# Kernel tuning notes

Measured on AMD Instinct MI355X. Metric: run time of the kernel, lower is better.

Reference implementation:

```python
import jax, jax.numpy as jnp
import numpy as np

N_NODES = 50000
N_EDGES = 1_600_000
IN_DIM = 256
OUT_DIM = 128
NEG_SLOPE = 0.01  # F.leaky_relu default


def setup_inputs() -> dict:
    key = jax.random.key(0)
    k1, k2, k3, k4, k5 = jax.random.split(key, 5)
    x = jax.random.normal(k1, (N_NODES, IN_DIM), dtype=jnp.float32)
    # glorot_init: uniform in [-r, r], r = sqrt(6/(in+out))
    r = np.sqrt(6.0 / (IN_DIM + OUT_DIM)).astype(np.float32)
    weight = jax.random.uniform(k2, (IN_DIM, OUT_DIM), dtype=jnp.float32, minval=-r, maxval=r)
    adj_rows = jax.random.randint(k3, (N_EDGES,), 0, N_NODES, dtype=jnp.int64 if jax.config.jax_enable_x64 else jnp.int32)
    adj_cols = jax.random.randint(k4, (N_EDGES,), 0, N_NODES, dtype=jnp.int64 if jax.config.jax_enable_x64 else jnp.int32)
    adj_vals = jax.random.uniform(k5, (N_EDGES,), dtype=jnp.float32)
    return {"x": x, "weight": weight, "adj_vals": adj_vals,
            "adj_rows": adj_rows, "adj_cols": adj_cols}


def reference(x, weight, adj_vals, adj_rows, adj_cols):
    # h = X @ W : [N, OUT_DIM]
    h = x @ weight
    # sparse adj @ h via edge-list SpMM: out[r] += v * h[c]
    msgs = adj_vals[:, None] * h[adj_cols]            # [E, OUT_DIM]
    agg = jax.ops.segment_sum(msgs, adj_rows, num_segments=N_NODES)
    # leaky_relu epilogue
    return jnp.where(agg >= 0, agg, NEG_SLOPE * agg)
```

## Files before the change

kernel.cpp:

```cpp
#include <hip/hip_runtime.h>
#include <hip/hip_fp16.h>

#define N_NODES 50000
#define N_EDGES 1600000
#define IN_DIM 256
#define OUT_DIM 128
#define NEG_SLOPE 0.01f

#define BIN_SH    7
#define BIN_ROWS  128
#define NBIN      ((N_NODES + BIN_ROWS - 1) / BIN_ROWS)
#define CAPB      4864

#define HIST_BLOCKS 512
#define CONVW_BLOCKS 16
#define EPB_H (N_EDGES / HIST_BLOCKS)
#define SCAT_BLOCKS 512
#define EPB_S (N_EDGES / SCAT_BLOCKS)
#define SCAT_ITERS ((EPB_S + 511) / 512)

typedef _Float16 f16x8 __attribute__((ext_vector_type(8)));
typedef float    f32x4 __attribute__((ext_vector_type(4)));
typedef float    f32x8 __attribute__((ext_vector_type(8)));

__device__ __forceinline__ float lrelu(float v) {
    return v >= 0.f ? v : NEG_SLOPE * v;
}

#define BM 128
#define GEMM_BLOCKS ((N_NODES + BM - 1) / BM)

#define CVT16(lo, hi) do { \
    lo[0]=(_Float16)xr[0].x; lo[1]=(_Float16)xr[0].y; lo[2]=(_Float16)xr[0].z; lo[3]=(_Float16)xr[0].w; \
    lo[4]=(_Float16)xr[1].x; lo[5]=(_Float16)xr[1].y; lo[6]=(_Float16)xr[1].z; lo[7]=(_Float16)xr[1].w; \
    hi[0]=(_Float16)xr[2].x; hi[1]=(_Float16)xr[2].y; hi[2]=(_Float16)xr[2].z; hi[3]=(_Float16)xr[2].w; \
    hi[4]=(_Float16)xr[3].x; hi[5]=(_Float16)xr[3].y; hi[6]=(_Float16)xr[3].z; hi[7]=(_Float16)xr[3].w; \
} while (0)

__global__ __launch_bounds__(256, 2) void gemm_xw_mfma(const float* __restrict__ x,
                                                       const __half* __restrict__ wtl,
                                                       __half* __restrict__ h) {
    __shared__ f16x8 wt8[32 * 128];
    __shared__ f16x8 xs8[2][4][BM];

    const int t    = threadIdx.x;
    const int lane = t & 63;
    const int wv   = t >> 6;
    const int row0 = blockIdx.x * BM;

    {
        const int4* src = (const int4*)wtl;
        int4* dst = (int4*)wt8;
#pragma unroll
        for (int i = 0; i < 16; ++i) dst[i * 256 + t] = src[i * 256 + t];
    }

    const int srow = t >> 1;
    const int skh  = t & 1;
    const int grow = row0 + srow;
    const bool rv  = grow < N_NODES;
    const float* xp = x + (size_t)(rv ? grow : 0) * IN_DIM + skh * 16;

    float4 xr[4];
#pragma unroll
    for (int i = 0; i < 4; ++i)
        xr[i] = rv ? ((const float4*)xp)[i] : make_float4(0.f, 0.f, 0.f, 0.f);
    {
        f16x8 lo, hi;
        CVT16(lo, hi);
        xs8[0][skh * 2 + 0][srow] = lo;
        xs8[0][skh * 2 + 1][srow] = hi;
    }
    __syncthreads();

    f32x4 acc[2][8];
#pragma unroll
    for (int mf = 0; mf < 2; ++mf)
#pragma unroll
        for (int nf = 0; nf < 8; ++nf) acc[mf][nf] = (f32x4){0.f, 0.f, 0.f, 0.f};

    const int kg  = lane >> 4;
    const int l15 = lane & 15;
    const int mb  = (wv << 5) + l15;

#pragma unroll
    for (int ks = 0; ks < 8; ++ks) {
        const int cur = ks & 1;
        if (ks < 7) {
#pragma unroll
            for (int i = 0; i < 4; ++i)
                xr[i] = rv ? ((const float4*)(xp + (ks + 1) * 32))[i]
                           : make_float4(0.f, 0.f, 0.f, 0.f);
        }
        const f16x8 b0 = xs8[cur][kg][mb];
        const f16x8 b1 = xs8[cur][kg][mb + 16];
#pragma unroll
        for (int nf = 0; nf < 8; ++nf) {
            const f16x8 a = wt8[(((ks << 2) | kg) << 7) + (nf << 4) + l15];
            acc[0][nf] = __builtin_amdgcn_mfma_f32_16x16x32_f16(a, b0, acc[0][nf], 0, 0, 0);
            acc[1][nf] = __builtin_amdgcn_mfma_f32_16x16x32_f16(a, b1, acc[1][nf], 0, 0, 0);
        }
        if (ks < 7) {
            f16x8 lo, hi;
            CVT16(lo, hi);
            xs8[cur ^ 1][skh * 2 + 0][srow] = lo;
            xs8[cur ^ 1][skh * 2 + 1][srow] = hi;
            __syncthreads();
        }
    }

    const int rg = lane >> 4;
#pragma unroll
    for (int mf = 0; mf < 2; ++mf) {
        const int m = row0 + (wv << 5) + (mf << 4) + l15;
        if (m < N_NODES) {
            __half* hp = h + (size_t)m * OUT_DIM + (rg << 2);
#pragma unroll
            for (int nf = 0; nf < 8; ++nf) {
                union { ushort4 u; __half f[4]; } o;
                o.f[0] = __float2half(acc[mf][nf][0]);
                o.f[1] = __float2half(acc[mf][nf][1]);
                o.f[2] = __float2half(acc[mf][nf][2]);
                o.f[3] = __float2half(acc[mf][nf][3]);
                *(ushort4*)(hp + (nf << 4)) = o.u;
            }
        }
    }
}

__global__ __launch_bounds__(256) void bucket_hist(const int* __restrict__ rows,
                                                   int* __restrict__ counts,
                                                   const float* __restrict__ w,
                                                   __half* __restrict__ wtl) {
    if (blockIdx.x >= HIST_BLOCKS) {
        const int e0 = ((blockIdx.x - HIST_BLOCKS) * 256 + threadIdx.x) * 8;
        const int k  = e0 >> 7;
        const int n0 = e0 & 127;
        const float4 a = *(const float4*)(w + e0);
        const float4 b = *(const float4*)(w + e0 + 4);
        __half* dst = wtl + ((size_t)((k >> 3) * 128 + n0)) * 8 + (k & 7);
        dst[0]  = __float2half(a.x);
        dst[8]  = __float2half(a.y);
        dst[16] = __float2half(a.z);
        dst[24] = __float2half(a.w);
        dst[32] = __float2half(b.x);
        dst[40] = __float2half(b.y);
        dst[48] = __float2half(b.z);
        dst[56] = __float2half(b.w);
        return;
    }

    __shared__ int lhist[NBIN];
    const int t = threadIdx.x;
    const int ebase = blockIdx.x * EPB_H;

    for (int b = t; b < NBIN; b += 256) lhist[b] = 0;
    __syncthreads();

    for (int k = 0; k < EPB_H; k += 256) {
        if (k + t < EPB_H) atomicAdd(&lhist[rows[ebase + k + t] >> BIN_SH], 1);
    }
    __syncthreads();

    for (int b = t; b < NBIN; b += 256) {
        const int c = lhist[b];
        if (c > 0) atomicAdd(&counts[b], c);
    }
}

__global__ __launch_bounds__(512) void scatter_bins(const int* __restrict__ rows,
                                                    const int* __restrict__ cols,
                                                    const float* __restrict__ vals,
                                                    const int* __restrict__ counts,
                                                    int* __restrict__ cursor,
                                                    int2* __restrict__ ebuf) {
    __shared__ int sb[512];
    __shared__ int lbase[NBIN];
    const int t = threadIdx.x;
    const int ebase = blockIdx.x * EPB_S;

    sb[t] = (t < NBIN) ? counts[t] : 0;
    const int myc = sb[t];
    __syncthreads();
    for (int off = 1; off < 512; off <<= 1) {
        const int u = (t >= off) ? sb[t - off] : 0;
        __syncthreads();
        sb[t] += u;
        __syncthreads();
    }
    if (t < NBIN) lbase[t] = sb[t] - myc;
    __syncthreads();
    if (t < NBIN) sb[t] = 0;
    __syncthreads();

    int myr[SCAT_ITERS];
#pragma unroll
    for (int k = 0; k < SCAT_ITERS; ++k) {
        const int i = k * 512 + t;
        myr[k] = -1;
        if (i < EPB_S) {
            const int r = rows[ebase + i];
            myr[k] = r;
            atomicAdd(&sb[r >> BIN_SH], 1);
        }
    }
    __syncthreads();

    if (t < NBIN) {
        const int c = sb[t];
        sb[t] = (c > 0) ? (lbase[t] + atomicAdd(&cursor[t], c)) : 0;
    }
    __syncthreads();

#pragma unroll
    for (int k = 0; k < SCAT_ITERS; ++k) {
        const int i = k * 512 + t;
        if (i < EPB_S) {
            const int e = ebase + i;
            const int r = myr[k];
            const int pos = atomicAdd(&sb[r >> BIN_SH], 1);
            ebuf[pos] = make_int2(cols[e] | ((r & (BIN_ROWS - 1)) << 16), __float_as_int(vals[e]));
        }
    }
}

__global__ __launch_bounds__(512) void sort_gather(const int* __restrict__ counts,
                                                   const int2* __restrict__ ebuf,
                                                   const __half* __restrict__ h,
                                                   float* __restrict__ out) {
    __shared__ int2 srec[CAPB];
    __shared__ int  hist[BIN_ROWS];
    __shared__ int  pfx[BIN_ROWS];
    __shared__ int  rowoff_l[BIN_ROWS + 1];
    __shared__ int  s_base, s_cnt;

    const int t   = threadIdx.x;
    const int bin = blockIdx.x;
    int* sb = (int*)srec;

    sb[t] = (t < NBIN) ? counts[t] : 0;
    const int myc = sb[t];
    __syncthreads();
    for (int off = 1; off < 512; off <<= 1) {
        const int u = (t >= off) ? sb[t - off] : 0;
        __syncthreads();
        sb[t] += u;
        __syncthreads();
    }
    if (t == bin) { s_base = sb[t] - myc; s_cnt = myc; }
    if (t < BIN_ROWS) hist[t] = 0;
    __syncthreads();
    const int base = s_base;
    const int cnt  = s_cnt;

    const int wv   = t >> 6;
    const int lane = t & 63;

    if (cnt <= CAPB) {
        for (int i = t; i < cnt; i += 512)
            atomicAdd(&hist[(ebuf[base + i].x >> 16) & (BIN_ROWS - 1)], 1);
        __syncthreads();

        if (t < BIN_ROWS) pfx[t] = hist[t];
        __syncthreads();
        for (int off = 1; off < BIN_ROWS; off <<= 1) {
            const int u = (t >= off && t < BIN_ROWS) ? pfx[t - off] : 0;
            __syncthreads();
            if (t < BIN_ROWS) pfx[t] += u;
            __syncthreads();
        }
        if (t < BIN_ROWS) {
            const int excl = pfx[t] - hist[t];
            rowoff_l[t] = excl;
            if (t == BIN_ROWS - 1) rowoff_l[BIN_ROWS] = cnt;
            hist[t] = excl;
        }
        __syncthreads();

        for (int i = t; i < cnt; i += 512) {
            const int2 r = ebuf[base + i];
            const int pos = atomicAdd(&hist[(r.x >> 16) & (BIN_ROWS - 1)], 1);
            srec[pos] = r;
        }
        __syncthreads();

        const int grp = lane >> 4;
        const int gl  = lane & 15;
        for (int rp = 0; rp < 8; ++rp) {
            const int lr0 = (wv << 4) + 2 * rp;
            const int lr1 = lr0 + 1;
            const int b0 = rowoff_l[lr0], e0 = rowoff_l[lr0 + 1];
            const int b1 = rowoff_l[lr1], e1 = rowoff_l[lr1 + 1];
            const int n0 = e0 - b0, n1 = e1 - b1;
            const int nmax = n0 > n1 ? n0 : n1;
            const int iters = (nmax + 3) >> 2;

            f32x8 a0 = (f32x8){0.f,0.f,0.f,0.f,0.f,0.f,0.f,0.f};
            f32x8 a1 = (f32x8){0.f,0.f,0.f,0.f,0.f,0.f,0.f,0.f};

            for (int it = 0; it < iters; ++it) {
                const int i0 = b0 + (it << 2) + grp;
                const int i1 = b1 + (it << 2) + grp;
                const bool v0i = i0 < e0;
                const bool v1i = i1 < e1;
                const int2 rA = srec[v0i ? i0 : 0];
                const int2 rB = srec[v1i ? i1 : 0];
                const float vA = v0i ? __int_as_float(rA.y) : 0.f;
                const float vB = v1i ? __int_as_float(rB.y) : 0.f;
                const f16x8 hA = *(const f16x8*)(h + (size_t)(rA.x & 0xFFFF) * OUT_DIM + (gl << 3));
                const f16x8 hB = *(const f16x8*)(h + (size_t)(rB.x & 0xFFFF) * OUT_DIM + (gl << 3));
#pragma unroll
                for (int j = 0; j < 8; ++j) {
                    a0[j] += vA * (float)hA[j];
                    a1[j] += vB * (float)hB[j];
                }
            }

#pragma unroll
            for (int j = 0; j < 8; ++j) {
                float x0 = a0[j], x1 = a1[j];
                x0 += __shfl_xor(x0, 16); x0 += __shfl_xor(x0, 32);
                x1 += __shfl_xor(x1, 16); x1 += __shfl_xor(x1, 32);
                a0[j] = x0; a1[j] = x1;
            }

            const int lrow = (grp & 2) ? lr1 : lr0;
            const int grow = (bin << BIN_SH) + lrow;
            float q[4];
#pragma unroll
            for (int k = 0; k < 4; ++k) {
                const float lo = (grp & 2) ? a1[k]     : a0[k];
                const float hi = (grp & 2) ? a1[k + 4] : a0[k + 4];
                q[k] = lrelu((grp & 1) ? hi : lo);
            }
            if (grow < N_NODES) {
                float4 o = make_float4(q[0], q[1], q[2], q[3]);
                *(float4*)(out + (size_t)grow * OUT_DIM + (gl << 3) + ((grp & 1) << 2)) = o;
            }
        }
    } else {
        for (int rr = 0; rr < 16; ++rr) {
            const int lr = (wv << 4) + rr;
            float2 acc = make_float2(0.f, 0.f);
            for (int e = 0; e < cnt; ++e) {
                const int2 rec = ebuf[base + e];
                if (((rec.x >> 16) & (BIN_ROWS - 1)) == lr) {
                    const float2 m = __half22float2(((const __half2*)(h + (size_t)(rec.x & 0xFFFF) * OUT_DIM))[lane]);
                    const float v = __int_as_float(rec.y);
                    acc.x += v * m.x; acc.y += v * m.y;
                }
            }
            const int grow = (bin << BIN_SH) + lr;
            if (grow < N_NODES) {
                acc.x = lrelu(acc.x); acc.y = lrelu(acc.y);
                ((float2*)(out + (size_t)grow * OUT_DIM))[lane] = acc;
            }
        }
    }
}

extern "C" void kernel_launch(void* const* d_in, const int* in_sizes, int n_in,
                              void* d_out, int out_size, void* d_ws, size_t ws_size,
                              hipStream_t stream) {
    const float* x    = (const float*)d_in[0];
    const float* w    = (const float*)d_in[1];
    const float* vals = (const float*)d_in[2];
    const int*   rows = (const int*)d_in[3];
    const int*   cols = (const int*)d_in[4];
    float* out = (float*)d_out;

    char* ws = (char*)d_ws;
    size_t off = 0;
    auto alloc = [&](size_t bytes) {
        void* p = ws + off;
        off = (off + bytes + 255) & ~(size_t)255;
        return p;
    };
    __half* h      = (__half*)alloc((size_t)N_NODES * OUT_DIM * sizeof(__half));
    int2*  ebuf    = (int2*) alloc((size_t)N_EDGES * sizeof(int2));
    __half* wtl    = (__half*)alloc((size_t)IN_DIM * OUT_DIM * sizeof(__half));
    int*   meta    = (int*)  alloc((size_t)(2 * NBIN) * sizeof(int));
    int*   counts  = meta;
    int*   cursor  = meta + NBIN;

    hipMemsetAsync(meta, 0, (size_t)(2 * NBIN) * sizeof(int), stream);

    bucket_hist<<<HIST_BLOCKS + CONVW_BLOCKS, 256, 0, stream>>>(rows, counts, w, wtl);
    gemm_xw_mfma<<<GEMM_BLOCKS, 256, 0, stream>>>(x, wtl, h);
    scatter_bins<<<SCAT_BLOCKS, 512, 0, stream>>>(rows, cols, vals, counts, cursor, ebuf);
    sort_gather<<<NBIN, 512, 0, stream>>>(counts, ebuf, h, out);
}
```

Before: 228.3 us.

## Replace histogram pass with fixed-capacity bins and overflow buffer, shrink bins

Drops the separate bucket histogram kernel by giving each bin a fixed-capacity slot region (CAPB records), so edges are scattered in one pass with per-bin atomic cursors and no global prefix scan. Bins shrink from 128 rows to 32 rows, which gives many more gather blocks, a smaller shared buffer and a wave-shuffle prefix scan. Records past the capacity go to a global overflow list that affected bins scan linearly. The cost is a larger padded workspace and a slow path if a bin overflows, which is unlikely for uniform random rows.

New measurement: 203.7 us. -10.8%, faster.

```diff
diff --git a/kernel.cpp b/kernel.cpp
--- a/kernel.cpp
+++ b/kernel.cpp
@@ -7,15 +7,14 @@
 #define OUT_DIM 128
 #define NEG_SLOPE 0.01f
 
-#define BIN_SH    7
-#define BIN_ROWS  128
+#define BIN_SH    5
+#define BIN_ROWS  32
 #define NBIN      ((N_NODES + BIN_ROWS - 1) / BIN_ROWS)
-#define CAPB      4864
-
-#define HIST_BLOCKS 512
-#define CONVW_BLOCKS 16
-#define EPB_H (N_EDGES / HIST_BLOCKS)
-#define SCAT_BLOCKS 512
+#define CAPB      1280
+#define OVF_CAP   65536
+
+#define SCAT_BLOCKS 256
+#define CONVW_BLOCKS 8
 #define EPB_S (N_EDGES / SCAT_BLOCKS)
 #define SCAT_ITERS ((EPB_S + 511) / 512)
 
@@ -128,12 +127,17 @@
     }
 }
 
-__global__ __launch_bounds__(256) void bucket_hist(const int* __restrict__ rows,
-                                                   int* __restrict__ counts,
-                                                   const float* __restrict__ w,
-                                                   __half* __restrict__ wtl) {
-    if (blockIdx.x >= HIST_BLOCKS) {
-        const int e0 = ((blockIdx.x - HIST_BLOCKS) * 256 + threadIdx.x) * 8;
+__global__ __launch_bounds__(512) void scatter_bins(const int* __restrict__ rows,
+                                                    const int* __restrict__ cols,
+                                                    const float* __restrict__ vals,
+                                                    int* __restrict__ cursor,
+                                                    int* __restrict__ ovfcnt,
+                                                    int2* __restrict__ ebuf,
+                                                    int2* __restrict__ ovfbuf,
+                                                    const float* __restrict__ w,
+                                                    __half* __restrict__ wtl) {
+    if (blockIdx.x >= SCAT_BLOCKS) {
+        const int e0 = ((blockIdx.x - SCAT_BLOCKS) * 512 + threadIdx.x) * 8;
         const int k  = e0 >> 7;
         const int n0 = e0 & 127;
         const float4 a = *(const float4*)(w + e0);
@@ -150,47 +154,11 @@
         return;
     }
 
-    __shared__ int lhist[NBIN];
-    const int t = threadIdx.x;
-    const int ebase = blockIdx.x * EPB_H;
-
-    for (int b = t; b < NBIN; b += 256) lhist[b] = 0;
-    __syncthreads();
-
-    for (int k = 0; k < EPB_H; k += 256) {
-        if (k + t < EPB_H) atomicAdd(&lhist[rows[ebase + k + t] >> BIN_SH], 1);
-    }
-    __syncthreads();
-
-    for (int b = t; b < NBIN; b += 256) {
-        const int c = lhist[b];
-        if (c > 0) atomicAdd(&counts[b], c);
-    }
-}
-
-__global__ __launch_bounds__(512) void scatter_bins(const int* __restrict__ rows,
-                                                    const int* __restrict__ cols,
-                                                    const float* __restrict__ vals,
-                                                    const int* __restrict__ counts,
-                                                    int* __restrict__ cursor,
-                                                    int2* __restrict__ ebuf) {
-    __shared__ int sb[512];
-    __shared__ int lbase[NBIN];
+    __shared__ int lcur[NBIN];
     const int t = threadIdx.x;
     const int ebase = blockIdx.x * EPB_S;
 
-    sb[t] = (t < NBIN) ? counts[t] : 0;
-    const int myc = sb[t];
-    __syncthreads();
-    for (int off = 1; off < 512; off <<= 1) {
-        const int u = (t >= off) ? sb[t - off] : 0;
-        __syncthreads();
-        sb[t] += u;
-        __syncthreads();
-    }
-    if (t < NBIN) lbase[t] = sb[t] - myc;
-    __syncthreads();
-    if (t < NBIN) sb[t] = 0;
+    for (int b = t; b < NBIN; b += 512) lcur[b] = 0;
     __syncthreads();
 
     int myr[SCAT_ITERS];
@@ -201,14 +169,14 @@
         if (i < EPB_S) {
             const int r = rows[ebase + i];
             myr[k] = r;
-            atomicAdd(&sb[r >> BIN_SH], 1);
-        }
-    }
-    __syncthreads();
-
-    if (t < NBIN) {
-        const int c = sb[t];
-        sb[t] = (c > 0) ? (lbase[t] + atomicAdd(&cursor[t], c)) : 0;
+            atomicAdd(&lcur[r >> BIN_SH], 1);
+        }
+    }
+    __syncthreads();
+
+    for (int b = t; b < NBIN; b += 512) {
+        const int c = lcur[b];
+        lcur[b] = (c > 0) ? atomicAdd(&cursor[b], c) : 0;
     }
     __syncthreads();
 
@@ -218,143 +186,137 @@
         if (i < EPB_S) {
             const int e = ebase + i;
             const int r = myr[k];
-            const int pos = atomicAdd(&sb[r >> BIN_SH], 1);
-            ebuf[pos] = make_int2(cols[e] | ((r & (BIN_ROWS - 1)) << 16), __float_as_int(vals[e]));
-        }
-    }
-}
-
-__global__ __launch_bounds__(512) void sort_gather(const int* __restrict__ counts,
+            const int bin = r >> BIN_SH;
+            const int off = atomicAdd(&lcur[bin], 1);
+            const int key = cols[e] | ((r & (BIN_ROWS - 1)) << 16);
+            const int vb  = __float_as_int(vals[e]);
+            if (off < CAPB) {
+                ebuf[(size_t)bin * CAPB + off] = make_int2(key, vb);
+            } else {
+                const int p = atomicAdd(ovfcnt, 1);
+                if (p < OVF_CAP) ovfbuf[p] = make_int2(key | (bin << 21), vb);
+            }
+        }
+    }
+}
+
+__global__ __launch_bounds__(512) void sort_gather(const int* __restrict__ cursor,
+                                                   const int* __restrict__ ovfcnt,
                                                    const int2* __restrict__ ebuf,
+                                                   const int2* __restrict__ ovfbuf,
                                                    const __half* __restrict__ h,
                                                    float* __restrict__ out) {
     __shared__ int2 srec[CAPB];
     __shared__ int  hist[BIN_ROWS];
-    __shared__ int  pfx[BIN_ROWS];
     __shared__ int  rowoff_l[BIN_ROWS + 1];
-    __shared__ int  s_base, s_cnt;
-
-    const int t   = threadIdx.x;
-    const int bin = blockIdx.x;
-    int* sb = (int*)srec;
-
-    sb[t] = (t < NBIN) ? counts[t] : 0;
-    const int myc = sb[t];
-    __syncthreads();
-    for (int off = 1; off < 512; off <<= 1) {
-        const int u = (t >= off) ? sb[t - off] : 0;
-        __syncthreads();
-        sb[t] += u;
-        __syncthreads();
-    }
-    if (t == bin) { s_base = sb[t] - myc; s_cnt = myc; }
-    if (t < BIN_ROWS) hist[t] = 0;
-    __syncthreads();
-    const int base = s_base;
-    const int cnt  = s_cnt;
-
+
+    const int t    = threadIdx.x;
+    const int bin  = blockIdx.x;
     const int wv   = t >> 6;
     const int lane = t & 63;
 
-    if (cnt <= CAPB) {
-        for (int i = t; i < cnt; i += 512)
-            atomicAdd(&hist[(ebuf[base + i].x >> 16) & (BIN_ROWS - 1)], 1);
-        __syncthreads();
-
-        if (t < BIN_ROWS) pfx[t] = hist[t];
-        __syncthreads();
+    const int cnt_all = cursor[bin];
+    const int cnt     = cnt_all < CAPB ? cnt_all : CAPB;
+    const size_t base = (size_t)bin * CAPB;
+
+    if (t < BIN_ROWS) hist[t] = 0;
+    __syncthreads();
+
+    for (int i = t; i < cnt; i += 512)
+        atomicAdd(&hist[(ebuf[base + i].x >> 16) & (BIN_ROWS - 1)], 1);
+    __syncthreads();
+
+    if (t < BIN_ROWS) {
+        const int v = hist[t];
+        int s = v;
+#pragma unroll
         for (int off = 1; off < BIN_ROWS; off <<= 1) {
-            const int u = (t >= off && t < BIN_ROWS) ? pfx[t - off] : 0;
-            __syncthreads();
-            if (t < BIN_ROWS) pfx[t] += u;
-            __syncthreads();
-        }
-        if (t < BIN_ROWS) {
-            const int excl = pfx[t] - hist[t];
-            rowoff_l[t] = excl;
-            if (t == BIN_ROWS - 1) rowoff_l[BIN_ROWS] = cnt;
-            hist[t] = excl;
-        }
-        __syncthreads();
-
-        for (int i = t; i < cnt; i += 512) {
-            const int2 r = ebuf[base + i];
-            const int pos = atomicAdd(&hist[(r.x >> 16) & (BIN_ROWS - 1)], 1);
-            srec[pos] = r;
-        }
-        __syncthreads();
-
-        const int grp = lane >> 4;
-        const int gl  = lane & 15;
-        for (int rp = 0; rp < 8; ++rp) {
-            const int lr0 = (wv << 4) + 2 * rp;
-            const int lr1 = lr0 + 1;
-            const int b0 = rowoff_l[lr0], e0 = rowoff_l[lr0 + 1];
-            const int b1 = rowoff_l[lr1], e1 = rowoff_l[lr1 + 1];
-            const int n0 = e0 - b0, n1 = e1 - b1;
-            const int nmax = n0 > n1 ? n0 : n1;
-            const int iters = (nmax + 3) >> 2;
-
-            f32x8 a0 = (f32x8){0.f,0.f,0.f,0.f,0.f,0.f,0.f,0.f};
-            f32x8 a1 = (f32x8){0.f,0.f,0.f,0.f,0.f,0.f,0.f,0.f};
-
-            for (int it = 0; it < iters; ++it) {
-                const int i0 = b0 + (it << 2) + grp;
-                const int i1 = b1 + (it << 2) + grp;
-                const bool v0i = i0 < e0;
-                const bool v1i = i1 < e1;
-                const int2 rA = srec[v0i ? i0 : 0];
-                const int2 rB = srec[v1i ? i1 : 0];
-                const float vA = v0i ? __int_as_float(rA.y) : 0.f;
-                const float vB = v1i ? __int_as_float(rB.y) : 0.f;
-                const f16x8 hA = *(const f16x8*)(h + (size_t)(rA.x & 0xFFFF) * OUT_DIM + (gl << 3));
-                const f16x8 hB = *(const f16x8*)(h + (size_t)(rB.x & 0xFFFF) * OUT_DIM + (gl << 3));
-#pragma unroll
-                for (int j = 0; j < 8; ++j) {
-                    a0[j] += vA * (float)hA[j];
-                    a1[j] += vB * (float)hB[j];
+            const int u = __shfl_up(s, off);
+            if (t >= off) s += u;
+        }
+        rowoff_l[t + 1] = s;
+        hist[t] = s - v;
+        if (t == 0) rowoff_l[0] = 0;
+    }
+    __syncthreads();
+
+    for (int i = t; i < cnt; i += 512) {
+        const int2 r = ebuf[base + i];
+        const int pos = atomicAdd(&hist[(r.x >> 16) & (BIN_ROWS - 1)], 1);
+        srec[pos] = r;
+    }
+    __syncthreads();
+
+    const int grp = lane >> 4;
+    const int gl  = lane & 15;
+    const int novf = (cnt_all > CAPB) ? *ovfcnt : 0;
+
+    for (int p = 0; p < 2; ++p) {
+        const int lr0 = (wv << 2) + 2 * p;
+        const int lr1 = lr0 + 1;
+        const int b0 = rowoff_l[lr0], e0 = rowoff_l[lr0 + 1];
+        const int b1 = rowoff_l[lr1], e1 = rowoff_l[lr1 + 1];
+        const int n0 = e0 - b0, n1 = e1 - b1;
+        const int nmax = n0 > n1 ? n0 : n1;
+        const int iters = (nmax + 3) >> 2;
+
+        f32x8 a0 = (f32x8){0.f,0.f,0.f,0.f,0.f,0.f,0.f,0.f};
+        f32x8 a1 = (f32x8){0.f,0.f,0.f,0.f,0.f,0.f,0.f,0.f};
+
+        for (int it = 0; it < iters; ++it) {
+            const int i0 = b0 + (it << 2) + grp;
+            const int i1 = b1 + (it << 2) + grp;
+            const bool v0i = i0 < e0;
+            const bool v1i = i1 < e1;
+            const int2 rA = srec[v0i ? i0 : 0];
+            const int2 rB = srec[v1i ? i1 : 0];
+            const float vA = v0i ? __int_as_float(rA.y) : 0.f;
+            const float vB = v1i ? __int_as_float(rB.y) : 0.f;
+            const f16x8 hA = *(const f16x8*)(h + (size_t)(rA.x & 0xFFFF) * OUT_DIM + (gl << 3));
+            const f16x8 hB = *(const f16x8*)(h + (size_t)(rB.x & 0xFFFF) * OUT_DIM + (gl << 3));
+#pragma unroll
+            for (int j = 0; j < 8; ++j) {
+                a0[j] += vA * (float)hA[j];
+                a1[j] += vB * (float)hB[j];
+            }
+        }
+
+        for (int e = 0; e < novf; ++e) {
+            const int2 rec = ovfbuf[e];
+            if ((rec.x >> 21) == bin && grp == 0) {
+                const int lrow = (rec.x >> 16) & (BIN_ROWS - 1);
+                if (lrow == lr0 || lrow == lr1) {
+                    const float v = __int_as_float(rec.y);
+                    const f16x8 hv = *(const f16x8*)(h + (size_t)(rec.x & 0xFFFF) * OUT_DIM + (gl << 3));
+#pragma unroll
+                    for (int j = 0; j < 8; ++j) {
+                        if (lrow == lr0) a0[j] += v * (float)hv[j];
+                        else             a1[j] += v * (float)hv[j];
+                    }
                 }
             }
-
-#pragma unroll
-            for (int j = 0; j < 8; ++j) {
-                float x0 = a0[j], x1 = a1[j];
-                x0 += __shfl_xor(x0, 16); x0 += __shfl_xor(x0, 32);
-                x1 += __shfl_xor(x1, 16); x1 += __shfl_xor(x1, 32);
-                a0[j] = x0; a1[j] = x1;
-            }
-
-            const int lrow = (grp & 2) ? lr1 : lr0;
-            const int grow = (bin << BIN_SH) + lrow;
-            float q[4];
-#pragma unroll
-            for (int k = 0; k < 4; ++k) {
-                const float lo = (grp & 2) ? a1[k]     : a0[k];
-                const float hi = (grp & 2) ? a1[k + 4] : a0[k + 4];
-                q[k] = lrelu((grp & 1) ? hi : lo);
-            }
-            if (grow < N_NODES) {
-                float4 o = make_float4(q[0], q[1], q[2], q[3]);
-                *(float4*)(out + (size_t)grow * OUT_DIM + (gl << 3) + ((grp & 1) << 2)) = o;
-            }
-        }
-    } else {
-        for (int rr = 0; rr < 16; ++rr) {
-            const int lr = (wv << 4) + rr;
-            float2 acc = make_float2(0.f, 0.f);
-            for (int e = 0; e < cnt; ++e) {
-                const int2 rec = ebuf[base + e];
-                if (((rec.x >> 16) & (BIN_ROWS - 1)) == lr) {
-                    const float2 m = __half22float2(((const __half2*)(h + (size_t)(rec.x & 0xFFFF) * OUT_DIM))[lane]);
-                    const float v = __int_as_float(rec.y);
-                    acc.x += v * m.x; acc.y += v * m.y;
-                }
-            }
-            const int grow = (bin << BIN_SH) + lr;
-            if (grow < N_NODES) {
-                acc.x = lrelu(acc.x); acc.y = lrelu(acc.y);
-                ((float2*)(out + (size_t)grow * OUT_DIM))[lane] = acc;
-            }
+        }
+
+#pragma unroll
+        for (int j = 0; j < 8; ++j) {
+            float x0 = a0[j], x1 = a1[j];
+            x0 += __shfl_xor(x0, 16); x0 += __shfl_xor(x0, 32);
+            x1 += __shfl_xor(x1, 16); x1 += __shfl_xor(x1, 32);
+            a0[j] = x0; a1[j] = x1;
+        }
+
+        const int lrow = (grp & 2) ? lr1 : lr0;
+        const int grow = (bin << BIN_SH) + lrow;
+        float q[4];
+#pragma unroll
+        for (int k = 0; k < 4; ++k) {
+            const float lo = (grp & 2) ? a1[k]     : a0[k];
+            const float hi = (grp & 2) ? a1[k + 4] : a0[k + 4];
+            q[k] = lrelu((grp & 1) ? hi : lo);
+        }
+        if (grow < N_NODES) {
+            float4 o = make_float4(q[0], q[1], q[2], q[3]);
+            *(float4*)(out + (size_t)grow * OUT_DIM + (gl << 3) + ((grp & 1) << 2)) = o;
         }
     }
 }
@@ -377,16 +339,17 @@
         return p;
     };
     __half* h      = (__half*)alloc((size_t)N_NODES * OUT_DIM * sizeof(__half));
-    int2*  ebuf    = (int2*) alloc((size_t)N_EDGES * sizeof(int2));
+    int2*  ebuf    = (int2*) alloc((size_t)NBIN * CAPB * sizeof(int2));
+    int2*  ovfbuf  = (int2*) alloc((size_t)OVF_CAP * sizeof(int2));
     __half* wtl    = (__half*)alloc((size_t)IN_DIM * OUT_DIM * sizeof(__half));
-    int*   meta    = (int*)  alloc((size_t)(2 * NBIN) * sizeof(int));
-    int*   counts  = meta;
-    int*   cursor  = meta + NBIN;
-
-    hipMemsetAsync(meta, 0, (size_t)(2 * NBIN) * sizeof(int), stream);
-
-    bucket_hist<<<HIST_BLOCKS + CONVW_BLOCKS, 256, 0, stream>>>(rows, counts, w, wtl);
+    int*   meta    = (int*)  alloc((size_t)(NBIN + 1) * sizeof(int));
+    int*   cursor  = meta;
+    int*   ovfcnt  = meta + NBIN;
+
+    hipMemsetAsync(meta, 0, (size_t)(NBIN + 1) * sizeof(int), stream);
+
+    scatter_bins<<<SCAT_BLOCKS + CONVW_BLOCKS, 512, 0, stream>>>(rows, cols, vals,
+                                                                 cursor, ovfcnt, ebuf, ovfbuf, w, wtl);
     gemm_xw_mfma<<<GEMM_BLOCKS, 256, 0, stream>>>(x, wtl, h);
-    scatter_bins<<<SCAT_BLOCKS, 512, 0, stream>>>(rows, cols, vals, counts, cursor, ebuf);
-    sort_gather<<<NBIN, 512, 0, stream>>>(counts, ebuf, h, out);
-}
+    sort_gather<<<NBIN, 512, 0, stream>>>(cursor, ovfcnt, ebuf, ovfbuf, h, out);
+}
```
